# Optimization experiments

Hardware: AMD Instinct MI355X
Metric: run time of the kernel (lower is better)

Reference implementation:

```python
import jax, jax.numpy as jnp
import numpy as np

D = 1024        # input_dim == hidden_dim (residual add requires equality)
NUM_CLASSES = 2
EPS = 1e-5      # torch LayerNorm default


def _layer_norm(x, gamma, beta):
    mu = jnp.mean(x, axis=-1, keepdims=True)
    var = jnp.var(x, axis=-1, keepdims=True)
    return (x - mu) * jax.lax.rsqrt(var + EPS) * gamma + beta


def setup_inputs() -> dict:
    key = jax.random.key(0)
    ks = jax.random.split(key, 16)
    B, S = 8, 2048
    s = 1.0 / np.sqrt(D)
    inp = {
        "x": jax.random.normal(ks[0], (B, S, D), dtype=jnp.float32),
        "Wq": jax.random.normal(ks[1], (D, D), dtype=jnp.float32) * s,
        "bq": jnp.zeros((D,), jnp.float32),
        "Wk": jax.random.normal(ks[2], (D, D), dtype=jnp.float32) * s,
        "bk": jnp.zeros((D,), jnp.float32),
        "Wv": jax.random.normal(ks[3], (D, D), dtype=jnp.float32) * s,
        "bv": jnp.zeros((D,), jnp.float32),
        "Wd": jax.random.normal(ks[4], (D, D), dtype=jnp.float32) * s,
        "bd": jnp.zeros((D,), jnp.float32),
        "g1": jnp.ones((D,), jnp.float32),
        "b1": jnp.zeros((D,), jnp.float32),
        "g2": jnp.ones((D,), jnp.float32),
        "b2": jnp.zeros((D,), jnp.float32),
        "Wc": jax.random.normal(ks[5], (D, NUM_CLASSES), dtype=jnp.float32) * s,
        "bc": jnp.zeros((NUM_CLASSES,), jnp.float32),
    }
    return inp


def reference(x, Wq, bq, Wk, bk, Wv, bv, Wd, bd, g1, b1, g2, b2, Wc, bc):
    # Q/K/V projections
    q = x @ Wq + bq                                   # [B,S,D]
    k = x @ Wk + bk
    v = x @ Wv + bv
    # scores scaled by sqrt(input_dim) (as in the original code)
    scores = jnp.einsum('bsd,btd->bst', q, k) / np.sqrt(D).astype(np.float32)
    attn = jax.nn.softmax(scores, axis=-1)            # [B,S,S]
    weighted = jnp.einsum('bst,btd->bsd', attn, v)    # [B,S,D]
    weighted = _layer_norm(weighted + x, g1, b1)
    h = jax.nn.relu(weighted @ Wd + bd)
    h = _layer_norm(h + weighted, g2, b2)
    # dropout is identity in eval mode
    logits = h[:, 0, :] @ Wc + bc                     # [B,num_classes]
    return logits
```

## Files before the change

### kernel.cpp

```cpp
#include <hip/hip_runtime.h>
#include <math.h>

#define B 8
#define S 2048
#define D 1024

#define UPART_OFF 0
#define NUMP_OFF  131072
#define DENP_OFF  1179648
#define WACC_OFF  1180672
#define HACC_OFF  1213440
#define U_OFF     1246208
#define ZERO_BEG  1180672
#define ZERO_CNT  65536

__device__ __forceinline__ float waveReduceSum(float v) {
#pragma unroll
    for (int k = 32; k >= 1; k >>= 1) v += __shfl_xor(v, k, 64);
    return v;
}
__device__ float blockReduceSum(float v) {
    __shared__ float sm[4];
    int lane = threadIdx.x & 63, wid = threadIdx.x >> 6;
    v = waveReduceSum(v);
    __syncthreads();
    if (lane == 0) sm[wid] = v;
    __syncthreads();
    return sm[0] + sm[1] + sm[2] + sm[3];
}

__global__ void __launch_bounds__(256) kA(const float* __restrict__ x,
                                          const float* __restrict__ Wq,
                                          const float* __restrict__ bq,
                                          const float* __restrict__ Wk,
                                          float* __restrict__ ws) {
    const int tid = threadIdx.x;
    for (int zi = blockIdx.x * 256 + tid; zi < ZERO_CNT; zi += 16384)
        ws[ZERO_BEG + zi] = 0.f;
    const int gi = blockIdx.x >> 2, hi = blockIdx.x & 3;
    __shared__ float xs[8][1024];
    __shared__ float4 zred4[16][8][16];
    __shared__ float zf[8][64];
    for (int jj = tid; jj < 2048; jj += 256) {
        int b = jj >> 8, off = jj & 255;
        ((float4*)xs[b])[off] = ((const float4*)(x + (size_t)b * S * D))[off];
    }
    __syncthreads();
    {
        const int jf = tid & 15, eg = tid >> 4;
        const float4* wq4 = (const float4*)Wq + gi * 16 + jf;
        const int e0 = eg * 64;
        float4 az[8];
#pragma unroll
        for (int b = 0; b < 8; ++b) az[b] = make_float4(0.f, 0.f, 0.f, 0.f);
#pragma unroll 8
        for (int e = 0; e < 64; ++e) {
            float4 w = wq4[(size_t)(e0 + e) * 256];
#pragma unroll
            for (int b = 0; b < 8; ++b) {
                float xv = xs[b][e0 + e];
                az[b].x += xv * w.x;
                az[b].y += xv * w.y;
                az[b].z += xv * w.z;
                az[b].w += xv * w.w;
            }
        }
#pragma unroll
        for (int b = 0; b < 8; ++b) zred4[eg][b][jf] = az[b];
    }
    __syncthreads();
    if (tid < 128) {
        int b = tid >> 4, jf = tid & 15;
        float4 s = make_float4(0.f, 0.f, 0.f, 0.f);
#pragma unroll
        for (int g = 0; g < 16; ++g) {
            float4 v = zred4[g][b][jf];
            s.x += v.x; s.y += v.y; s.z += v.z; s.w += v.w;
        }
        float4 bb = ((const float4*)bq)[gi * 16 + jf];
        zf[b][jf * 4 + 0] = s.x + bb.x;
        zf[b][jf * 4 + 1] = s.y + bb.y;
        zf[b][jf * 4 + 2] = s.z + bb.z;
        zf[b][jf * 4 + 3] = s.w + bb.w;
    }
    __syncthreads();
    {
        const int d = hi * 256 + tid;
        const float4* wk4 = (const float4*)(Wk + (size_t)d * D + gi * 64);
        float au[8] = {0.f, 0.f, 0.f, 0.f, 0.f, 0.f, 0.f, 0.f};
#pragma unroll
        for (int jq = 0; jq < 16; ++jq) {
            float4 w4 = wk4[jq];
#pragma unroll
            for (int b = 0; b < 8; ++b)
                au[b] += w4.x * zf[b][jq * 4 + 0] + w4.y * zf[b][jq * 4 + 1] +
                         w4.z * zf[b][jq * 4 + 2] + w4.w * zf[b][jq * 4 + 3];
        }
#pragma unroll
        for (int b = 0; b < 8; ++b)
            ws[UPART_OFF + (((size_t)gi * 8 + b) << 10) + d] = au[b];
    }
}

__global__ void __launch_bounds__(128) kU(float* __restrict__ ws) {
    const int b = blockIdx.x >> 1, half = blockIdx.x & 1;
    const int f4 = half * 128 + threadIdx.x;
    const float4* up4 = (const float4*)(ws + UPART_OFF);
    float4 s = make_float4(0.f, 0.f, 0.f, 0.f);
#pragma unroll
    for (int g = 0; g < 16; ++g) {
        float4 v = up4[(g * 8 + b) * 256 + f4];
        s.x += v.x; s.y += v.y; s.z += v.z; s.w += v.w;
    }
    ((float4*)(ws + U_OFF))[b * 256 + f4] = s;
}

__global__ void __launch_bounds__(256) kB(const float* __restrict__ x,
                                          float* __restrict__ ws) {
    const int b = blockIdx.y;
    const int bx = blockIdx.x;
    const int t0 = bx * 16;
    const int tid = threadIdx.x;
    const int wave = tid >> 6, lane = tid & 63;
    const float4* xb4 = (const float4*)(x + (size_t)b * S * D);
    float4 uv = ((const float4*)(ws + U_OFF))[b * 256 + tid];
    float4 xr[16];
#pragma unroll
    for (int t = 0; t < 16; ++t) xr[t] = xb4[(size_t)(t0 + t) * 256 + tid];
    __shared__ float part[16][256];
#pragma unroll
    for (int t = 0; t < 16; ++t)
        part[t][tid] = xr[t].x * uv.x + xr[t].y * uv.y + xr[t].z * uv.z + xr[t].w * uv.w;
    __syncthreads();
    __shared__ float s_sc[16];
#pragma unroll
    for (int r = 0; r < 4; ++r) {
        int t = wave * 4 + r;
        float v = part[t][lane] + part[t][lane + 64] + part[t][lane + 128] + part[t][lane + 192];
        v = waveReduceSum(v);
        if (lane == 0) s_sc[t] = v * 0.03125f;
    }
    __syncthreads();
    float p[16], l = 0.f;
#pragma unroll
    for (int t = 0; t < 16; ++t) {
        p[t] = __expf(s_sc[t]);
        l += p[t];
    }
    float4 wl = {0.f, 0.f, 0.f, 0.f};
#pragma unroll
    for (int t = 0; t < 16; ++t) {
        wl.x += p[t] * xr[t].x;
        wl.y += p[t] * xr[t].y;
        wl.z += p[t] * xr[t].z;
        wl.w += p[t] * xr[t].w;
    }
    ((float4*)(ws + NUMP_OFF + (size_t)(bx * 8 + b) * 1024))[tid] = wl;
    if (tid == 0) ws[DENP_OFF + bx * 8 + b] = l;
}

__global__ void __launch_bounds__(256) kC(const float* __restrict__ Wv,
                                          float* __restrict__ ws) {
    const int tid = threadIdx.x;
    const int bid = blockIdx.x;
    const int d0 = (bid >> 2) * 32;
    const int dp = (bid & 3) * 256 + tid;
    const int c = (bid >> 2) & 3;
    __shared__ float dsm[1024], invden[8], vs[8][32];
    for (int j = tid; j < 1024; j += 256) dsm[j] = ws[DENP_OFF + j];
    __syncthreads();
    if (tid < 8) {
        float s = 0.f;
        for (int pp = 0; pp < 128; ++pp) s += dsm[pp * 8 + tid];
        invden[tid] = 1.f / s;
    }
    __syncthreads();
    {
        int b = tid >> 5, dd = tid & 31;
        float s = 0.f;
#pragma unroll 16
        for (int pp = 0; pp < 128; ++pp)
            s += ws[NUMP_OFF + (size_t)(pp * 8 + b) * 1024 + d0 + dd];
        vs[b][dd] = s * invden[b];
    }
    __syncthreads();
    float acc[8] = {0.f, 0.f, 0.f, 0.f, 0.f, 0.f, 0.f, 0.f};
#pragma unroll 8
    for (int dd = 0; dd < 32; ++dd) {
        float wv = Wv[(size_t)(d0 + dd) * D + dp];
#pragma unroll
        for (int b = 0; b < 8; ++b) acc[b] += vs[b][dd] * wv;
    }
#pragma unroll
    for (int b = 0; b < 8; ++b)
        atomicAdd(ws + WACC_OFF + (size_t)c * 8192 + b * 1024 + dp, acc[b]);
}

__global__ void __launch_bounds__(256) kD(const float* __restrict__ bv,
                                          const float* __restrict__ x,
                                          const float* __restrict__ g1,
                                          const float* __restrict__ b1,
                                          const float* __restrict__ Wd,
                                          float* __restrict__ ws) {
    const int tid = threadIdx.x;
    const int bid = blockIdx.x;
    const int d0 = (bid >> 2) * 32;
    const int dp = (bid & 3) * 256 + tid;
    const int c2 = (bid >> 2) & 3;
    const int wave = tid >> 6, lane = tid & 63;
    __shared__ float sMu[8], sInv[8], vs[8][32];
    {
        const float4* wacc4 = (const float4*)(ws + WACC_OFF);
        const float4* bv4 = (const float4*)bv;
#pragma unroll
        for (int h = 0; h < 2; ++h) {
            int b = wave + h * 4;
            const float4* xb4r = (const float4*)(x + (size_t)b * S * D);
            float s = 0.f, ss = 0.f;
#pragma unroll
            for (int i = 0; i < 4; ++i) {
                int idx = lane + 64 * i;
                float4 wv = wacc4[0 * 2048 + b * 256 + idx];
                float4 w1 = wacc4[1 * 2048 + b * 256 + idx];
                float4 w2 = wacc4[2 * 2048 + b * 256 + idx];
                float4 w3 = wacc4[3 * 2048 + b * 256 + idx];
                float4 bb = bv4[idx];
                float4 xv = xb4r[idx];
                float v0 = wv.x + w1.x + w2.x + w3.x + bb.x + xv.x;
                float v1 = wv.y + w1.y + w2.y + w3.y + bb.y + xv.y;
                float v2 = wv.z + w1.z + w2.z + w3.z + bb.z + xv.z;
                float v3 = wv.w + w1.w + w2.w + w3.w + bb.w + xv.w;
                s += v0 + v1 + v2 + v3;
                ss += v0 * v0 + v1 * v1 + v2 * v2 + v3 * v3;
            }
            s = waveReduceSum(s);
            ss = waveReduceSum(ss);
            if (lane == 0) {
                float mu = s * (1.0f / D);
                sMu[b] = mu;
                sInv[b] = rsqrtf(ss * (1.0f / D) - mu * mu + 1e-5f);
            }
        }
    }
    __syncthreads();
    {
        int b = tid >> 5, dd = tid & 31, d = d0 + dd;
        float v = ws[WACC_OFF + 0 * 8192 + b * 1024 + d] +
                  ws[WACC_OFF + 1 * 8192 + b * 1024 + d] +
                  ws[WACC_OFF + 2 * 8192 + b * 1024 + d] +
                  ws[WACC_OFF + 3 * 8192 + b * 1024 + d] +
                  bv[d] + x[(size_t)b * S * D + d];
        vs[b][dd] = (v - sMu[b]) * sInv[b] * g1[d] + b1[d];
    }
    __syncthreads();
    float acc[8] = {0.f, 0.f, 0.f, 0.f, 0.f, 0.f, 0.f, 0.f};
#pragma unroll 8
    for (int dd = 0; dd < 32; ++dd) {
        float wv = Wd[(size_t)(d0 + dd) * D + dp];
#pragma unroll
        for (int b = 0; b < 8; ++b) acc[b] += vs[b][dd] * wv;
    }
#pragma unroll
    for (int b = 0; b < 8; ++b)
        atomicAdd(ws + HACC_OFF + (size_t)c2 * 8192 + b * 1024 + dp, acc[b]);
}

__global__ void __launch_bounds__(256) kE(const float* __restrict__ bv,
                                          const float* __restrict__ x,
                                          const float* __restrict__ g1,
                                          const float* __restrict__ b1,
                                          const float* __restrict__ bd,
                                          const float* __restrict__ g2,
                                          const float* __restrict__ b2,
                                          const float* __restrict__ Wc,
                                          const float* __restrict__ bc,
                                          const float* __restrict__ ws,
                                          float* __restrict__ out) {
    const int b = blockIdx.x;
    const int tid = threadIdx.x;
    const float4* wacc4 = (const float4*)(ws + WACC_OFF);
    const float4* hacc4 = (const float4*)(ws + HACC_OFF);
    float4 w0 = wacc4[0 * 2048 + b * 256 + tid];
    float4 w1 = wacc4[1 * 2048 + b * 256 + tid];
    float4 w2 = wacc4[2 * 2048 + b * 256 + tid];
    float4 w3 = wacc4[3 * 2048 + b * 256 + tid];
    float4 h0 = hacc4[0 * 2048 + b * 256 + tid];
    float4 h1 = hacc4[1 * 2048 + b * 256 + tid];
    float4 h2 = hacc4[2 * 2048 + b * 256 + tid];
    float4 h3 = hacc4[3 * 2048 + b * 256 + tid];
    float4 bb = ((const float4*)bv)[tid];
    float4 xv = ((const float4*)(x + (size_t)b * S * D))[tid];
    float4 g14 = ((const float4*)g1)[tid];
    float4 b14 = ((const float4*)b1)[tid];
    float4 bd4 = ((const float4*)bd)[tid];
    float4 g24 = ((const float4*)g2)[tid];
    float4 b24 = ((const float4*)b2)[tid];
    float4 wc0 = ((const float4*)Wc)[tid * 2];
    float4 wc1 = ((const float4*)Wc)[tid * 2 + 1];
    float4 r;
    r.x = w0.x + w1.x + w2.x + w3.x + bb.x + xv.x;
    r.y = w0.y + w1.y + w2.y + w3.y + bb.y + xv.y;
    r.z = w0.z + w1.z + w2.z + w3.z + bb.z + xv.z;
    r.w = w0.w + w1.w + w2.w + w3.w + bb.w + xv.w;
    float s = blockReduceSum(r.x + r.y + r.z + r.w);
    float ss = blockReduceSum(r.x * r.x + r.y * r.y + r.z * r.z + r.w * r.w);
    float mu1 = s * (1.0f / D);
    float inv1 = rsqrtf(ss * (1.0f / D) - mu1 * mu1 + 1e-5f);
    float4 hs;
    hs.x = fmaxf(h0.x + h1.x + h2.x + h3.x + bd4.x, 0.f) + (r.x - mu1) * inv1 * g14.x + b14.x;
    hs.y = fmaxf(h0.y + h1.y + h2.y + h3.y + bd4.y, 0.f) + (r.y - mu1) * inv1 * g14.y + b14.y;
    hs.z = fmaxf(h0.z + h1.z + h2.z + h3.z + bd4.z, 0.f) + (r.z - mu1) * inv1 * g14.z + b14.z;
    hs.w = fmaxf(h0.w + h1.w + h2.w + h3.w + bd4.w, 0.f) + (r.w - mu1) * inv1 * g14.w + b14.w;
    float s2 = blockReduceSum(hs.x + hs.y + hs.z + hs.w);
    float ss2 = blockReduceSum(hs.x * hs.x + hs.y * hs.y + hs.z * hs.z + hs.w * hs.w);
    float mu2 = s2 * (1.0f / D);
    float inv2 = rsqrtf(ss2 * (1.0f / D) - mu2 * mu2 + 1e-5f);
    float l0 = (hs.x - mu2) * inv2 * g24.x + b24.x;
    float l1 = (hs.y - mu2) * inv2 * g24.y + b24.y;
    float l2v = (hs.z - mu2) * inv2 * g24.z + b24.z;
    float l3 = (hs.w - mu2) * inv2 * g24.w + b24.w;
    float p0 = blockReduceSum(l0 * wc0.x + l1 * wc0.z + l2v * wc1.x + l3 * wc1.z);
    float p1 = blockReduceSum(l0 * wc0.y + l1 * wc0.w + l2v * wc1.y + l3 * wc1.w);
    if (tid == 0) {
        out[b * 2 + 0] = p0 + bc[0];
        out[b * 2 + 1] = p1 + bc[1];
    }
}

extern "C" void kernel_launch(void* const* d_in, const int* in_sizes, int n_in,
                              void* d_out, int out_size, void* d_ws, size_t ws_size,
                              hipStream_t stream) {
    const float* x  = (const float*)d_in[0];
    const float* Wq = (const float*)d_in[1];
    const float* bq = (const float*)d_in[2];
    const float* Wk = (const float*)d_in[3];
    const float* Wv = (const float*)d_in[5];
    const float* bv = (const float*)d_in[6];
    const float* Wd = (const float*)d_in[7];
    const float* bd = (const float*)d_in[8];
    const float* g1 = (const float*)d_in[9];
    const float* b1 = (const float*)d_in[10];
    const float* g2 = (const float*)d_in[11];
    const float* b2 = (const float*)d_in[12];
    const float* Wc = (const float*)d_in[13];
    const float* bc = (const float*)d_in[14];
    float* out = (float*)d_out;
    float* ws = (float*)d_ws;

    kA<<<64, 256, 0, stream>>>(x, Wq, bq, Wk, ws);
    kU<<<16, 128, 0, stream>>>(ws);
    kB<<<dim3(128, 8), 256, 0, stream>>>(x, ws);
    kC<<<128, 256, 0, stream>>>(Wv, ws);
    kD<<<128, 256, 0, stream>>>(bv, x, g1, b1, Wd, ws);
    kE<<<8, 256, 0, stream>>>(bv, x, g1, b1, bd, g2, b2, Wc, bc, ws, out);
}
```

Baseline: 161.0 us.

## Restructure q·Wk^T pipeline, vectorize numerator reduction, hoist LayerNorm stats

The fused kA/kU pair becomes two kernels. kZ computes z = x0·Wq + bq with a column-tiled split-K scheme and an in-block two-level reduction. kW then computes u = Wk·z with one wave per output row, which removes the 16-way partial buffer and the separate reduction kernel. kC now sums the 128 numerator partials with float4 loads spread across four wave groups instead of scalar strided loads. The per-batch LayerNorm mean and inverse std move out of every kD block into a tiny kS kernel, so 128 blocks no longer recompute them, at the cost of one more launch.

```diff
diff --git a/kernel.cpp b/kernel.cpp
--- a/kernel.cpp
+++ b/kernel.cpp
@@ -5,13 +5,15 @@
 #define S 2048
 #define D 1024
 
-#define UPART_OFF 0
-#define NUMP_OFF  131072
-#define DENP_OFF  1179648
-#define WACC_OFF  1180672
-#define HACC_OFF  1213440
-#define U_OFF     1246208
-#define ZERO_BEG  1180672
+#define Z_OFF     0
+#define U_OFF     8192
+#define NUMP_OFF  16384
+#define DENP_OFF  1064960
+#define WACC_OFF  1065984
+#define HACC_OFF  1098752
+#define SMU_OFF   1131520
+#define SINV_OFF  1131528
+#define ZERO_BEG  1065984
 #define ZERO_CNT  65536
 
 __device__ __forceinline__ float waveReduceSum(float v) {
@@ -29,90 +31,99 @@
     return sm[0] + sm[1] + sm[2] + sm[3];
 }
 
-__global__ void __launch_bounds__(256) kA(const float* __restrict__ x,
+__global__ void __launch_bounds__(256) kZ(const float* __restrict__ x,
                                           const float* __restrict__ Wq,
                                           const float* __restrict__ bq,
-                                          const float* __restrict__ Wk,
-                                          float* __restrict__ ws) {
-    const int tid = threadIdx.x;
-    for (int zi = blockIdx.x * 256 + tid; zi < ZERO_CNT; zi += 16384)
-        ws[ZERO_BEG + zi] = 0.f;
-    const int gi = blockIdx.x >> 2, hi = blockIdx.x & 3;
+                                          float* __restrict__ ws) {
+    const int tid = threadIdx.x;
+    {
+        int zi = blockIdx.x * 256 + tid;
+#pragma unroll
+        for (int r = 0; r < 4; ++r) ws[ZERO_BEG + zi + r * 16384] = 0.f;
+    }
+    float* z = ws + Z_OFF;
+    const int dp0 = blockIdx.x * 16;
+    const int dpf = tid & 3;
+    const int kg = tid >> 2;
     __shared__ float xs[8][1024];
-    __shared__ float4 zred4[16][8][16];
-    __shared__ float zf[8][64];
-    for (int jj = tid; jj < 2048; jj += 256) {
-        int b = jj >> 8, off = jj & 255;
+    __shared__ float4 redB[8 * 4 * 8];
+    for (int j = tid; j < 2048; j += 256) {
+        int b = j >> 8, off = j & 255;
         ((float4*)xs[b])[off] = ((const float4*)(x + (size_t)b * S * D))[off];
     }
     __syncthreads();
+    const float4* Wq4 = (const float4*)Wq + (dp0 >> 2) + dpf;
+    float4 acc4[8];
+#pragma unroll
+    for (int b = 0; b < 8; ++b) acc4[b] = make_float4(0.f, 0.f, 0.f, 0.f);
+    const int k0 = kg * 16;
+#pragma unroll
+    for (int i = 0; i < 16; ++i) {
+        int k = k0 + i;
+        float4 w4 = Wq4[(size_t)k * 256];
+#pragma unroll
+        for (int b = 0; b < 8; ++b) {
+            float xv = xs[b][k];
+            acc4[b].x += xv * w4.x;
+            acc4[b].y += xv * w4.y;
+            acc4[b].z += xv * w4.z;
+            acc4[b].w += xv * w4.w;
+        }
+    }
+    __syncthreads();
+    float4* redA = (float4*)xs;
+#pragma unroll
+    for (int b = 0; b < 8; ++b) redA[(kg * 4 + dpf) * 8 + b] = acc4[b];
+    __syncthreads();
     {
-        const int jf = tid & 15, eg = tid >> 4;
-        const float4* wq4 = (const float4*)Wq + gi * 16 + jf;
-        const int e0 = eg * 64;
-        float4 az[8];
-#pragma unroll
-        for (int b = 0; b < 8; ++b) az[b] = make_float4(0.f, 0.f, 0.f, 0.f);
-#pragma unroll 8
-        for (int e = 0; e < 64; ++e) {
-            float4 w = wq4[(size_t)(e0 + e) * 256];
-#pragma unroll
-            for (int b = 0; b < 8; ++b) {
-                float xv = xs[b][e0 + e];
-                az[b].x += xv * w.x;
-                az[b].y += xv * w.y;
-                az[b].z += xv * w.z;
-                az[b].w += xv * w.w;
-            }
-        }
-#pragma unroll
-        for (int b = 0; b < 8; ++b) zred4[eg][b][jf] = az[b];
-    }
-    __syncthreads();
-    if (tid < 128) {
-        int b = tid >> 4, jf = tid & 15;
+        int b = tid & 7, dpf2 = (tid >> 3) & 3, kh = tid >> 5;
         float4 s = make_float4(0.f, 0.f, 0.f, 0.f);
 #pragma unroll
-        for (int g = 0; g < 16; ++g) {
-            float4 v = zred4[g][b][jf];
+        for (int g = 0; g < 8; ++g) {
+            float4 v = redA[((kh * 8 + g) * 4 + dpf2) * 8 + b];
             s.x += v.x; s.y += v.y; s.z += v.z; s.w += v.w;
         }
-        float4 bb = ((const float4*)bq)[gi * 16 + jf];
-        zf[b][jf * 4 + 0] = s.x + bb.x;
-        zf[b][jf * 4 + 1] = s.y + bb.y;
-        zf[b][jf * 4 + 2] = s.z + bb.z;
-        zf[b][jf * 4 + 3] = s.w + bb.w;
-    }
-    __syncthreads();
-    {
-        const int d = hi * 256 + tid;
-        const float4* wk4 = (const float4*)(Wk + (size_t)d * D + gi * 64);
-        float au[8] = {0.f, 0.f, 0.f, 0.f, 0.f, 0.f, 0.f, 0.f};
-#pragma unroll
-        for (int jq = 0; jq < 16; ++jq) {
-            float4 w4 = wk4[jq];
-#pragma unroll
-            for (int b = 0; b < 8; ++b)
-                au[b] += w4.x * zf[b][jq * 4 + 0] + w4.y * zf[b][jq * 4 + 1] +
-                         w4.z * zf[b][jq * 4 + 2] + w4.w * zf[b][jq * 4 + 3];
-        }
-#pragma unroll
-        for (int b = 0; b < 8; ++b)
-            ws[UPART_OFF + (((size_t)gi * 8 + b) << 10) + d] = au[b];
-    }
-}
-
-__global__ void __launch_bounds__(128) kU(float* __restrict__ ws) {
-    const int b = blockIdx.x >> 1, half = blockIdx.x & 1;
-    const int f4 = half * 128 + threadIdx.x;
-    const float4* up4 = (const float4*)(ws + UPART_OFF);
-    float4 s = make_float4(0.f, 0.f, 0.f, 0.f);
-#pragma unroll
-    for (int g = 0; g < 16; ++g) {
-        float4 v = up4[(g * 8 + b) * 256 + f4];
-        s.x += v.x; s.y += v.y; s.z += v.z; s.w += v.w;
-    }
-    ((float4*)(ws + U_OFF))[b * 256 + f4] = s;
+        redB[(kh * 4 + dpf2) * 8 + b] = s;
+    }
+    __syncthreads();
+    if (tid < 32) {
+        int b = tid & 7, dpf2 = tid >> 3;
+        float4 s = make_float4(0.f, 0.f, 0.f, 0.f);
+#pragma unroll
+        for (int g = 0; g < 8; ++g) {
+            float4 v = redB[(g * 4 + dpf2) * 8 + b];
+            s.x += v.x; s.y += v.y; s.z += v.z; s.w += v.w;
+        }
+        const float4 bb = ((const float4*)bq)[(dp0 >> 2) + dpf2];
+        float4 o;
+        o.x = s.x + bb.x; o.y = s.y + bb.y; o.z = s.z + bb.z; o.w = s.w + bb.w;
+        ((float4*)(z + (size_t)b * D + dp0))[dpf2] = o;
+    }
+}
+
+__global__ void __launch_bounds__(256) kW(const float* __restrict__ Wk,
+                                          float* __restrict__ ws) {
+    const float* z = ws + Z_OFF;
+    float* u = ws + U_OFF;
+    int wid = (blockIdx.x * 256 + threadIdx.x) >> 6;
+    int lane = threadIdx.x & 63;
+    const float4* Wk4 = (const float4*)(Wk + (size_t)wid * D);
+    const float4* z4 = (const float4*)z;
+    float acc[8] = {0.f, 0.f, 0.f, 0.f, 0.f, 0.f, 0.f, 0.f};
+#pragma unroll
+    for (int i = 0; i < 4; ++i) {
+        float4 wv = Wk4[lane + 64 * i];
+#pragma unroll
+        for (int b = 0; b < 8; ++b) {
+            float4 qv = z4[b * 256 + lane + 64 * i];
+            acc[b] += wv.x * qv.x + wv.y * qv.y + wv.z * qv.z + wv.w * qv.w;
+        }
+    }
+#pragma unroll
+    for (int b = 0; b < 8; ++b) {
+        float v = waveReduceSum(acc[b]);
+        if (lane == 0) u[b * D + wid] = v;
+    }
 }
 
 __global__ void __launch_bounds__(256) kB(const float* __restrict__ x,
@@ -167,7 +178,22 @@
     const int dp = (bid & 3) * 256 + tid;
     const int c = (bid >> 2) & 3;
     __shared__ float dsm[1024], invden[8], vs[8][32];
+    __shared__ float4 red4[4][64];
     for (int j = tid; j < 1024; j += 256) dsm[j] = ws[DENP_OFF + j];
+    {
+        const int f4o = tid & 63, pg = tid >> 6;
+        const int b = f4o >> 3, f8 = f4o & 7;
+        const float4* np4 = (const float4*)(ws + NUMP_OFF);
+        const size_t base = (size_t)(d0 >> 2) + f8;
+        float4 s4 = make_float4(0.f, 0.f, 0.f, 0.f);
+#pragma unroll 8
+        for (int i = 0; i < 32; ++i) {
+            int pp = pg * 32 + i;
+            float4 v = np4[(size_t)(pp * 8 + b) * 256 + base];
+            s4.x += v.x; s4.y += v.y; s4.z += v.z; s4.w += v.w;
+        }
+        red4[pg][f4o] = s4;
+    }
     __syncthreads();
     if (tid < 8) {
         float s = 0.f;
@@ -175,13 +201,15 @@
         invden[tid] = 1.f / s;
     }
     __syncthreads();
-    {
-        int b = tid >> 5, dd = tid & 31;
-        float s = 0.f;
-#pragma unroll 16
-        for (int pp = 0; pp < 128; ++pp)
-            s += ws[NUMP_OFF + (size_t)(pp * 8 + b) * 1024 + d0 + dd];
-        vs[b][dd] = s * invden[b];
+    if (tid < 64) {
+        float4 a0 = red4[0][tid], a1 = red4[1][tid];
+        float4 a2 = red4[2][tid], a3 = red4[3][tid];
+        int b2 = tid >> 3, f82 = tid & 7;
+        float inv = invden[b2];
+        vs[b2][f82 * 4 + 0] = (a0.x + a1.x + a2.x + a3.x) * inv;
+        vs[b2][f82 * 4 + 1] = (a0.y + a1.y + a2.y + a3.y) * inv;
+        vs[b2][f82 * 4 + 2] = (a0.z + a1.z + a2.z + a3.z) * inv;
+        vs[b2][f82 * 4 + 3] = (a0.w + a1.w + a2.w + a3.w) * inv;
     }
     __syncthreads();
     float acc[8] = {0.f, 0.f, 0.f, 0.f, 0.f, 0.f, 0.f, 0.f};
@@ -194,6 +222,32 @@
 #pragma unroll
     for (int b = 0; b < 8; ++b)
         atomicAdd(ws + WACC_OFF + (size_t)c * 8192 + b * 1024 + dp, acc[b]);
+}
+
+__global__ void __launch_bounds__(256) kS(const float* __restrict__ bv,
+                                          const float* __restrict__ x,
+                                          float* __restrict__ ws) {
+    const int b = blockIdx.x;
+    const int tid = threadIdx.x;
+    const float4* wacc4 = (const float4*)(ws + WACC_OFF);
+    float4 w0 = wacc4[0 * 2048 + b * 256 + tid];
+    float4 w1 = wacc4[1 * 2048 + b * 256 + tid];
+    float4 w2 = wacc4[2 * 2048 + b * 256 + tid];
+    float4 w3 = wacc4[3 * 2048 + b * 256 + tid];
+    float4 bb = ((const float4*)bv)[tid];
+    float4 xv = ((const float4*)(x + (size_t)b * S * D))[tid];
+    float4 r;
+    r.x = w0.x + w1.x + w2.x + w3.x + bb.x + xv.x;
+    r.y = w0.y + w1.y + w2.y + w3.y + bb.y + xv.y;
+    r.z = w0.z + w1.z + w2.z + w3.z + bb.z + xv.z;
+    r.w = w0.w + w1.w + w2.w + w3.w + bb.w + xv.w;
+    float s = blockReduceSum(r.x + r.y + r.z + r.w);
+    float ss = blockReduceSum(r.x * r.x + r.y * r.y + r.z * r.z + r.w * r.w);
+    if (tid == 0) {
+        float mu = s * (1.0f / D);
+        ws[SMU_OFF + b] = mu;
+        ws[SINV_OFF + b] = rsqrtf(ss * (1.0f / D) - mu * mu + 1e-5f);
+    }
 }
 
 __global__ void __launch_bounds__(256) kD(const float* __restrict__ bv,
@@ -207,40 +261,10 @@
     const int d0 = (bid >> 2) * 32;
     const int dp = (bid & 3) * 256 + tid;
     const int c2 = (bid >> 2) & 3;
-    const int wave = tid >> 6, lane = tid & 63;
     __shared__ float sMu[8], sInv[8], vs[8][32];
-    {
-        const float4* wacc4 = (const float4*)(ws + WACC_OFF);
-        const float4* bv4 = (const float4*)bv;
-#pragma unroll
-        for (int h = 0; h < 2; ++h) {
-            int b = wave + h * 4;
-            const float4* xb4r = (const float4*)(x + (size_t)b * S * D);
-            float s = 0.f, ss = 0.f;
-#pragma unroll
-            for (int i = 0; i < 4; ++i) {
-                int idx = lane + 64 * i;
-                float4 wv = wacc4[0 * 2048 + b * 256 + idx];
-                float4 w1 = wacc4[1 * 2048 + b * 256 + idx];
-                float4 w2 = wacc4[2 * 2048 + b * 256 + idx];
-                float4 w3 = wacc4[3 * 2048 + b * 256 + idx];
-                float4 bb = bv4[idx];
-                float4 xv = xb4r[idx];
-                float v0 = wv.x + w1.x + w2.x + w3.x + bb.x + xv.x;
-                float v1 = wv.y + w1.y + w2.y + w3.y + bb.y + xv.y;
-                float v2 = wv.z + w1.z + w2.z + w3.z + bb.z + xv.z;
-                float v3 = wv.w + w1.w + w2.w + w3.w + bb.w + xv.w;
-                s += v0 + v1 + v2 + v3;
-                ss += v0 * v0 + v1 * v1 + v2 * v2 + v3 * v3;
-            }
-            s = waveReduceSum(s);
-            ss = waveReduceSum(ss);
-            if (lane == 0) {
-                float mu = s * (1.0f / D);
-                sMu[b] = mu;
-                sInv[b] = rsqrtf(ss * (1.0f / D) - mu * mu + 1e-5f);
-            }
-        }
+    if (tid < 8) {
+        sMu[tid] = ws[SMU_OFF + tid];
+        sInv[tid] = ws[SINV_OFF + tid];
     }
     __syncthreads();
     {
@@ -347,10 +371,11 @@
     float* out = (float*)d_out;
     float* ws = (float*)d_ws;
 
-    kA<<<64, 256, 0, stream>>>(x, Wq, bq, Wk, ws);
-    kU<<<16, 128, 0, stream>>>(ws);
+    kZ<<<64, 256, 0, stream>>>(x, Wq, bq, ws);
+    kW<<<256, 256, 0, stream>>>(Wk, ws);
     kB<<<dim3(128, 8), 256, 0, stream>>>(x, ws);
     kC<<<128, 256, 0, stream>>>(Wv, ws);
+    kS<<<8, 256, 0, stream>>>(bv, x, ws);
     kD<<<128, 256, 0, stream>>>(bv, x, g1, b1, Wd, ws);
     kE<<<8, 256, 0, stream>>>(bv, x, g1, b1, bd, g2, b2, Wc, bc, ws, out);
 }
```

After: 152.9 us. 5.0% less time.
